# Kernel optimization log

Hardware: AMD Instinct MI355X
Metric: run time of the kernel (lower is better)

The kernel has to match this reference:

```python
import jax, jax.numpy as jnp
import numpy as np

NUM_HEADS = 16
HIDDEN = 1024
HEAD_DIM = HIDDEN // NUM_HEADS


def setup_inputs() -> dict:
    key = jax.random.key(0)
    ks = jax.random.split(key, 9)
    B, S, D = 2, 2048, HIDDEN
    s = 1.0 / np.sqrt(D)
    return {
        "x": jax.random.normal(ks[0], (B, S, D), dtype=jnp.float32),
        "Wq": jax.random.normal(ks[1], (D, D), dtype=jnp.float32) * s,
        "bq": jnp.zeros((D,), dtype=jnp.float32),
        "Wk": jax.random.normal(ks[2], (D, D), dtype=jnp.float32) * s,
        "bk": jnp.zeros((D,), dtype=jnp.float32),
        "Wv": jax.random.normal(ks[3], (D, D), dtype=jnp.float32) * s,
        "bv": jnp.zeros((D,), dtype=jnp.float32),
        "Wo": jax.random.normal(ks[4], (D, D), dtype=jnp.float32) * s,
        "bo": jnp.zeros((D,), dtype=jnp.float32),
    }


def reference(x, Wq, bq, Wk, bk, Wv, bv, Wo, bo):
    B, S, D = x.shape
    H, Hd = NUM_HEADS, HEAD_DIM
    # projections -> [B, H, S, Hd]
    def proj(W, b):
        return (x @ W + b).reshape(B, S, H, Hd).transpose(0, 2, 1, 3)
    q = proj(Wq, bq)
    k = proj(Wk, bk)
    v = proj(Wv, bv)
    scores = jnp.einsum('bhqd,bhkd->bhqk', q, k) / jnp.sqrt(jnp.float32(Hd))
    p_attn = jax.nn.softmax(scores, axis=-1)  # dropout = identity (eval)
    ctx = jnp.einsum('bhqk,bhkd->bhqd', p_attn, v)
    attn_mean = jnp.mean(p_attn, axis=1)  # [B, S, S]
    out = ctx.transpose(0, 2, 1, 3).reshape(B, S, D) @ Wo + bo
    return out, attn_mean
```

## Files before the change

kernel.cpp:

```cpp
#include <hip/hip_runtime.h>
#include <math.h>

#define NUM_HEADS 16
#define HEAD_DIM  64
#define HIDDEN    1024
#define BATCH     2
#define SEQ       2048

#define QSCALE 0.1803368801111204f

typedef short bf16x8 __attribute__((ext_vector_type(8)));
typedef short short4v __attribute__((ext_vector_type(4)));
typedef float f32x4 __attribute__((ext_vector_type(4)));

#if __has_builtin(__builtin_amdgcn_exp2f)
#define EXP2F __builtin_amdgcn_exp2f
#else
#define EXP2F exp2f
#endif

#define ACQB(N) do { asm volatile("s_waitcnt vmcnt(" #N ")" ::: "memory"); \
                     __builtin_amdgcn_s_barrier(); } while (0)
#define RELB()  do { asm volatile("s_waitcnt lgkmcnt(0)" ::: "memory");   \
                     __builtin_amdgcn_sched_barrier(0);                    \
                     __builtin_amdgcn_s_barrier(); } while (0)

__device__ __forceinline__ short f2bf(float f) {
    union { float f; unsigned int u; } x; x.f = f;
    unsigned int r = x.u + 0x7fffu + ((x.u >> 16) & 1u);
    return (short)(r >> 16);
}

__device__ __forceinline__ unsigned int pack_bf16_trunc(float lo, float hi) {
    return __builtin_amdgcn_perm(__float_as_uint(hi), __float_as_uint(lo), 0x07060302u);
}

__device__ __forceinline__ void async16(const void* g, void* l) {
    __builtin_amdgcn_global_load_lds(
        (const __attribute__((address_space(1))) void*)g,
        (__attribute__((address_space(3))) void*)l, 16, 0, 0);
}

__global__ __launch_bounds__(256)
void prep_kernel(const float* __restrict__ x,
                 const float* __restrict__ Wq, const float* __restrict__ Wk,
                 const float* __restrict__ Wv, const float* __restrict__ Wo,
                 short* __restrict__ xb, short* __restrict__ Wt4)
{
    __shared__ float t[64][65];
    const int tid = threadIdx.x;
    const int bid = blockIdx.x;
    if (bid < 4096) {
        size_t i = ((size_t)bid * 256 + tid) * 4;
        float4 v = *(const float4*)&x[i];
        short4v o;
        o.x = f2bf(v.x); o.y = f2bf(v.y); o.z = f2bf(v.z); o.w = f2bf(v.w);
        *(short4v*)&xb[i] = o;
        return;
    }
    const int tb = bid - 4096;
    const int z  = tb >> 8;
    const int cx = tb & 15, cy = (tb >> 4) & 15;
    const float* W = (z == 0) ? Wq : (z == 1) ? Wk : (z == 2) ? Wv : Wo;
    short* dst = Wt4 + (size_t)z * HIDDEN * HIDDEN;
    const int c0 = cx * 64;
    const int r0 = cy * 64;
    const int cl = tid & 63, rw = tid >> 6;
    #pragma unroll
    for (int p = 0; p < 16; ++p) {
        int row = p * 4 + rw;
        t[row][cl] = W[(size_t)(r0 + row) * HIDDEN + c0 + cl];
    }
    __syncthreads();
    #pragma unroll
    for (int p = 0; p < 16; ++p) {
        int orow = p * 4 + rw;
        dst[(size_t)(c0 + orow) * HIDDEN + r0 + cl] = f2bf(t[cl][orow]);
    }
}

__global__ __launch_bounds__(256)
void qkv_proj_kernel(const short* __restrict__ xb, const short* __restrict__ Wt4,
                     const float* __restrict__ bq, const float* __restrict__ bk,
                     const float* __restrict__ bv,
                     short* __restrict__ Qb, short* __restrict__ Kb,
                     short* __restrict__ Vt)
{
    __shared__ short ldsA[2][128 * 32];
    __shared__ short ldsB[2][128 * 32];
    const int tid = threadIdx.x;
    const int lane = tid & 63, w = tid >> 6;
    const int l = lane & 15, q = lane >> 4;
    const int n0 = blockIdx.x * 128;
    const int m0 = blockIdx.y * 128;
    const int z  = blockIdx.z;
    const short* Wt = Wt4 + (size_t)z * HIDDEN * HIDDEN;
    const int wm = (w >> 1) * 64, wn = (w & 1) * 64;
    const int kc = q ^ ((l >> 1) & 3);

    f32x4 acc[4][4];
    #pragma unroll
    for (int i = 0; i < 4; ++i)
        #pragma unroll
        for (int j = 0; j < 4; ++j)
            acc[i][j] = (f32x4){0.f, 0.f, 0.f, 0.f};

    auto STG = [&](int buf, int t) {
        #pragma unroll
        for (int half = 0; half < 2; ++half) {
            int c = half * 256 + tid;
            int row = c >> 2;
            int kcg = (c & 3) ^ ((row >> 1) & 3);
            async16(xb + (size_t)(m0 + row) * HIDDEN + t * 32 + kcg * 8, &ldsA[buf][c * 8]);
            async16(Wt + (size_t)(n0 + row) * HIDDEN + t * 32 + kcg * 8, &ldsB[buf][c * 8]);
        }
    };
    auto CMP = [&](int buf) {
        bf16x8 af[4], bfr[4];
        #pragma unroll
        for (int i = 0; i < 4; ++i)
            af[i] = *(const bf16x8*)&ldsA[buf][((wm + 16 * i + l) * 4 + kc) * 8];
        #pragma unroll
        for (int j = 0; j < 4; ++j)
            bfr[j] = *(const bf16x8*)&ldsB[buf][((wn + 16 * j + l) * 4 + kc) * 8];
        #pragma unroll
        for (int i = 0; i < 4; ++i)
            #pragma unroll
            for (int j = 0; j < 4; ++j)
                acc[i][j] = __builtin_amdgcn_mfma_f32_16x16x32_bf16(
                    af[i], bfr[j], acc[i][j], 0, 0, 0);
    };

    STG(0, 0); STG(1, 1);
    ACQB(4);
    for (int tp = 0; tp < 15; ++tp) {
        CMP(0); RELB(); STG(0, 2 * tp + 2); ACQB(4);
        CMP(1); RELB(); STG(1, 2 * tp + 3); ACQB(4);
    }
    CMP(0); RELB(); ACQB(0);
    CMP(1);

    const float* bias = (z == 0) ? bq : (z == 1) ? bk : bv;
    const float sc = (z == 0) ? QSCALE : 1.0f;
    if (z < 2) {
        short* Ob = (z == 0) ? Qb : Kb;
        #pragma unroll
        for (int j = 0; j < 4; ++j) {
            int n = n0 + wn + 16 * j + l;
            float bval = bias[n];
            int h = n >> 6, hd = n & 63;
            #pragma unroll
            for (int i = 0; i < 4; ++i) {
                #pragma unroll
                for (int reg = 0; reg < 4; ++reg) {
                    int m = m0 + wm + 16 * i + 4 * q + reg;
                    int b_ = m >> 11, s = m & 2047;
                    Ob[(((size_t)(b_ * NUM_HEADS + h) * SEQ) + s) * HEAD_DIM + hd] =
                        f2bf((acc[i][j][reg] + bval) * sc);
                }
            }
        }
    } else {
        #pragma unroll
        for (int j = 0; j < 4; ++j) {
            int n = n0 + wn + 16 * j + l;
            float bval = bias[n];
            int h = n >> 6, hd = n & 63;
            #pragma unroll
            for (int i = 0; i < 4; ++i) {
                int mb = m0 + wm + 16 * i + 4 * q;
                int b_ = mb >> 11, s = mb & 2047;
                short4v pk;
                #pragma unroll
                for (int reg = 0; reg < 4; ++reg)
                    pk[reg] = f2bf(acc[i][j][reg] + bval);
                *(short4v*)&Vt[(((size_t)(b_ * NUM_HEADS + h) * HEAD_DIM) + hd) * SEQ + s] = pk;
            }
        }
    }
}

__global__ __launch_bounds__(256)
void out_proj_kernel(const short* __restrict__ Cb, const short* __restrict__ Wot,
                     const float* __restrict__ bo, float* __restrict__ out)
{
    __shared__ short ldsA[2][64 * 32];
    __shared__ short ldsB[2][128 * 32];
    const int tid = threadIdx.x;
    const int lane = tid & 63, w = tid >> 6;
    const int l = lane & 15, q = lane >> 4;
    const int n0 = blockIdx.x * 128;
    const int m0 = blockIdx.y * 64;
    const int kc = q ^ ((l >> 1) & 3);

    f32x4 acc[4][2];
    #pragma unroll
    for (int i = 0; i < 4; ++i)
        #pragma unroll
        for (int j = 0; j < 2; ++j)
            acc[i][j] = (f32x4){0.f, 0.f, 0.f, 0.f};

    auto STG = [&](int buf, int t) {
        {
            int c = tid;
            int row = c >> 2;
            int kcg = (c & 3) ^ ((row >> 1) & 3);
            int m = m0 + row;
            int b_ = m >> 11, s = m & 2047;
            int h = t >> 1, hdb = (t & 1) << 5;
            async16(Cb + (((size_t)(b_ * NUM_HEADS + h) * SEQ) + s) * HEAD_DIM + hdb + kcg * 8,
                    &ldsA[buf][c * 8]);
        }
        #pragma unroll
        for (int half = 0; half < 2; ++half) {
            int c = half * 256 + tid;
            int row = c >> 2;
            int kcg = (c & 3) ^ ((row >> 1) & 3);
            async16(Wot + (size_t)(n0 + row) * HIDDEN + t * 32 + kcg * 8, &ldsB[buf][c * 8]);
        }
    };
    auto CMP = [&](int buf) {
        bf16x8 af[4], bfr[2];
        #pragma unroll
        for (int i = 0; i < 4; ++i)
            af[i] = *(const bf16x8*)&ldsA[buf][((16 * i + l) * 4 + kc) * 8];
        #pragma unroll
        for (int j = 0; j < 2; ++j)
            bfr[j] = *(const bf16x8*)&ldsB[buf][((32 * w + 16 * j + l) * 4 + kc) * 8];
        #pragma unroll
        for (int i = 0; i < 4; ++i)
            #pragma unroll
            for (int j = 0; j < 2; ++j)
                acc[i][j] = __builtin_amdgcn_mfma_f32_16x16x32_bf16(
                    af[i], bfr[j], acc[i][j], 0, 0, 0);
    };

    STG(0, 0); STG(1, 1);
    ACQB(3);
    for (int tp = 0; tp < 15; ++tp) {
        CMP(0); RELB(); STG(0, 2 * tp + 2); ACQB(3);
        CMP(1); RELB(); STG(1, 2 * tp + 3); ACQB(3);
    }
    CMP(0); RELB(); ACQB(0);
    CMP(1);

    #pragma unroll
    for (int j = 0; j < 2; ++j) {
        int n = n0 + 32 * w + 16 * j + l;
        float bval = bo[n];
        #pragma unroll
        for (int i = 0; i < 4; ++i)
            #pragma unroll
            for (int reg = 0; reg < 4; ++reg) {
                int m = m0 + 16 * i + 4 * q + reg;
                out[(size_t)m * HIDDEN + n] = acc[i][j][reg] + bval;
            }
    }
}

__global__ __launch_bounds__(512, 4)
void flash_kernel(const short* __restrict__ Qb, const short* __restrict__ Kb,
                  const short* __restrict__ Vt, short* __restrict__ Cb,
                  float* __restrict__ Lb)
{
    __shared__ short Ks[2][64 * 64];
    __shared__ short Vs[2][64 * 64];
    __shared__ float Xch[4][64][35];

    const int tid = threadIdx.x, lane = tid & 63, w = tid >> 6;
    const int l = lane & 15, q = lane >> 4;
    const int qg = w & 3;
    const int kh = w >> 2;
    const int q0 = blockIdx.x * 128;
    const int Q0 = q0 + qg * 32;
    const int h = blockIdx.y, b = blockIdx.z;
    const size_t base  = (size_t)(b * NUM_HEADS + h) * SEQ * HEAD_DIM;
    const size_t vbase = (size_t)(b * NUM_HEADS + h) * HEAD_DIM * SEQ;

    bf16x8 bq[2][2];
    #pragma unroll
    for (int u = 0; u < 2; ++u)
        #pragma unroll
        for (int ks = 0; ks < 2; ++ks)
            bq[u][ks] = *(const bf16x8*)(Qb + base +
                (size_t)(Q0 + 16 * u + l) * HEAD_DIM + 32 * ks + 8 * q);

    const int c = tid;
    const int row = c >> 3;
    const int g = ((c & 7) ^ (row & 7)) * 8;
    const short* kp = Kb + base + (size_t)row * HEAD_DIM + g;
    const short* vp = Vt + vbase + (size_t)row * SEQ + g;

    const int sw = l & 7;
    int kaddr[2];
    #pragma unroll
    for (int ks = 0; ks < 2; ++ks)
        kaddr[ks] = (32 * kh + l) * 64 + ((4 * ks + q) ^ sw) * 8;
    const int vc0 = 4 * kh + (q >> 1);
    const int vaddr0 = l * 64 + ((vc0      ^ sw) * 8) + 4 * (q & 1);
    const int vaddr1 = l * 64 + (((vc0 + 2) ^ sw) * 8) + 4 * (q & 1);

    f32x4 ctx[2][4];
    #pragma unroll
    for (int u = 0; u < 2; ++u)
        #pragma unroll
        for (int m = 0; m < 4; ++m) ctx[u][m] = (f32x4){0.f, 0.f, 0.f, 0.f};
    float l_part[2] = {0.f, 0.f};

    auto STG = [&](int buf) {
        async16(kp, &Ks[buf][c * 8]);
        async16(vp, &Vs[buf][c * 8]);
        kp += 64 * HEAD_DIM;
        vp += 64;
    };
    auto CMP = [&](int buf) {
        f32x4 st[2][2];
        #pragma unroll
        for (int u = 0; u < 2; ++u)
            #pragma unroll
            for (int t = 0; t < 2; ++t) st[u][t] = (f32x4){0.f, 0.f, 0.f, 0.f};
        #pragma unroll
        for (int ks = 0; ks < 2; ++ks) {
            #pragma unroll
            for (int t = 0; t < 2; ++t) {
                bf16x8 ak = *(const bf16x8*)&Ks[buf][kaddr[ks] + t * 1024];
                st[0][t] = __builtin_amdgcn_mfma_f32_16x16x32_bf16(ak, bq[0][ks], st[0][t], 0, 0, 0);
                st[1][t] = __builtin_amdgcn_mfma_f32_16x16x32_bf16(ak, bq[1][ks], st[1][t], 0, 0, 0);
            }
        }
        union { unsigned int u32[4]; bf16x8 v; } bp[2];
        #pragma unroll
        for (int u = 0; u < 2; ++u) {
            #pragma unroll
            for (int t = 0; t < 2; ++t) {
                float p0 = EXP2F(st[u][t][0]);
                float p1 = EXP2F(st[u][t][1]);
                float p2 = EXP2F(st[u][t][2]);
                float p3 = EXP2F(st[u][t][3]);
                l_part[u] += (p0 + p1) + (p2 + p3);
                bp[u].u32[2 * t]     = pack_bf16_trunc(p0, p1);
                bp[u].u32[2 * t + 1] = pack_bf16_trunc(p2, p3);
            }
        }
        #pragma unroll
        for (int m = 0; m < 4; ++m) {
            short4v g0 = *(const short4v*)&Vs[buf][vaddr0 + m * 1024];
            short4v g1 = *(const short4v*)&Vs[buf][vaddr1 + m * 1024];
            bf16x8 av = __builtin_shufflevector(g0, g1, 0, 1, 2, 3, 4, 5, 6, 7);
            ctx[0][m] = __builtin_amdgcn_mfma_f32_16x16x32_bf16(av, bp[0].v, ctx[0][m], 0, 0, 0);
            ctx[1][m] = __builtin_amdgcn_mfma_f32_16x16x32_bf16(av, bp[1].v, ctx[1][m], 0, 0, 0);
        }
    };

    STG(0); STG(1);
    ACQB(2);
    for (int tp = 0; tp < 15; ++tp) {
        CMP(0); RELB(); STG(0); ACQB(2);
        CMP(1); RELB(); STG(1); ACQB(2);
    }
    CMP(0); RELB(); ACQB(0);
    CMP(1);

    if (kh == 1) {
        float* dst = &Xch[qg][lane][0];
        #pragma unroll
        for (int u = 0; u < 2; ++u)
            #pragma unroll
            for (int m = 0; m < 4; ++m)
                #pragma unroll
                for (int r = 0; r < 4; ++r)
                    dst[u * 16 + m * 4 + r] = ctx[u][m][r];
        dst[32] = l_part[0];
        dst[33] = l_part[1];
    }
    __syncthreads();
    if (kh == 0) {
        const float* src = &Xch[qg][lane][0];
        #pragma unroll
        for (int u = 0; u < 2; ++u)
            #pragma unroll
            for (int m = 0; m < 4; ++m)
                #pragma unroll
                for (int r = 0; r < 4; ++r)
                    ctx[u][m][r] += src[u * 16 + m * 4 + r];

        #pragma unroll
        for (int u = 0; u < 2; ++u) {
            float rs = l_part[u] + src[32 + u];
            rs += __shfl_xor(rs, 16);
            rs += __shfl_xor(rs, 32);
            float inv_l = 1.0f / rs;
            int s = Q0 + 16 * u + l;
            #pragma unroll
            for (int t = 0; t < 4; ++t) {
                short4v pk;
                #pragma unroll
                for (int reg = 0; reg < 4; ++reg)
                    pk[reg] = f2bf(ctx[u][t][reg] * inv_l);
                *(short4v*)&Cb[(((size_t)(b * NUM_HEADS + h) * SEQ) + s) * HEAD_DIM + 16 * t + 4 * q] = pk;
            }
            if (q == 0)
                Lb[(size_t)(b * NUM_HEADS + h) * SEQ + s] = inv_l;
        }
    }
}

__global__ __launch_bounds__(256)
void attn_mean_kernel(const short* __restrict__ Qb, const short* __restrict__ Kb,
                      const float* __restrict__ Lb, float* __restrict__ amean)
{
    __shared__ short Qs[2][64 * 64];
    __shared__ short Ks[2][128 * 64];
    const int tid = threadIdx.x, lane = tid & 63, w = tid >> 6;
    const int l = lane & 15, q = lane >> 4;
    const int k0 = blockIdx.x * 128;
    const int q0 = blockIdx.y * 64;
    const int b  = blockIdx.z;
    const size_t HSTRIDE = (size_t)SEQ * HEAD_DIM;

    const short* qp[2];
    const short* kp[4];
    {
        const size_t base0 = (size_t)(b * NUM_HEADS) * HSTRIDE;
        #pragma unroll
        for (int i = 0; i < 2; ++i) {
            int cc = 256 * i + tid;
            int row = cc >> 3;
            int gg = ((cc & 7) ^ (row & 7)) * 8;
            qp[i] = Qb + base0 + (size_t)(q0 + row) * HEAD_DIM + gg;
        }
        #pragma unroll
        for (int i = 0; i < 4; ++i) {
            int cc = 256 * i + tid;
            int row = cc >> 3;
            int gg = ((cc & 7) ^ (row & 7)) * 8;
            kp[i] = Kb + base0 + (size_t)(k0 + row) * HEAD_DIM + gg;
        }
    }

    f32x4 macc[2][4];
    #pragma unroll
    for (int tk = 0; tk < 2; ++tk)
        #pragma unroll
        for (int tq = 0; tq < 4; ++tq)
            macc[tk][tq] = (f32x4){0.f, 0.f, 0.f, 0.f};

    auto STG = [&](int buf) {
        #pragma unroll
        for (int i = 0; i < 2; ++i) { async16(qp[i], &Qs[buf][(256 * i + tid) * 8]); qp[i] += HSTRIDE; }
        #pragma unroll
        for (int i = 0; i < 4; ++i) { async16(kp[i], &Ks[buf][(256 * i + tid) * 8]); kp[i] += HSTRIDE; }
    };
    int hc = 0;
    auto CMP = [&](int buf) {
        int h = hc++;
        float linv[4];
        #pragma unroll
        for (int tq = 0; tq < 4; ++tq)
            linv[tq] = Lb[(size_t)(b * NUM_HEADS + h) * SEQ + q0 + 16 * tq + l];

        bf16x8 bq[4][2];
        #pragma unroll
        for (int tq = 0; tq < 4; ++tq)
            #pragma unroll
            for (int ks = 0; ks < 2; ++ks) {
                int cc = (4 * ks + q) ^ (l & 7);
                bq[tq][ks] = *(const bf16x8*)&Qs[buf][((16 * tq + l) * 8 + cc) * 8];
            }
        #pragma unroll
        for (int tk = 0; tk < 2; ++tk) {
            bf16x8 ak[2];
            #pragma unroll
            for (int ks = 0; ks < 2; ++ks) {
                int cc = (4 * ks + q) ^ (l & 7);
                ak[ks] = *(const bf16x8*)&Ks[buf][((32 * w + 16 * tk + l) * 8 + cc) * 8];
            }
            #pragma unroll
            for (int tq = 0; tq < 4; ++tq) {
                f32x4 st = (f32x4){0.f, 0.f, 0.f, 0.f};
                st = __builtin_amdgcn_mfma_f32_16x16x32_bf16(ak[0], bq[tq][0], st, 0, 0, 0);
                st = __builtin_amdgcn_mfma_f32_16x16x32_bf16(ak[1], bq[tq][1], st, 0, 0, 0);
                float li = linv[tq];
                #pragma unroll
                for (int reg = 0; reg < 4; ++reg)
                    macc[tk][tq][reg] += EXP2F(st[reg]) * li;
            }
        }
    };

    STG(0); STG(1);
    ACQB(6);
    for (int tp = 0; tp < 7; ++tp) {
        CMP(0); RELB(); STG(0); ACQB(6);
        CMP(1); RELB(); STG(1); ACQB(6);
    }
    CMP(0); RELB(); ACQB(0);
    CMP(1);

    const float inv_h = 1.0f / (float)NUM_HEADS;
    #pragma unroll
    for (int tq = 0; tq < 4; ++tq) {
        int row_q = q0 + 16 * tq + l;
        #pragma unroll
        for (int tk = 0; tk < 2; ++tk) {
            int col_k = k0 + 32 * w + 16 * tk + 4 * q;
            f32x4 o;
            #pragma unroll
            for (int reg = 0; reg < 4; ++reg) o[reg] = macc[tk][tq][reg] * inv_h;
            *(f32x4*)&amean[((size_t)b * SEQ + row_q) * SEQ + col_k] = o;
        }
    }
}

extern "C" void kernel_launch(void* const* d_in, const int* in_sizes, int n_in,
                              void* d_out, int out_size, void* d_ws, size_t ws_size,
                              hipStream_t stream)
{
    const float* x  = (const float*)d_in[0];
    const float* Wq = (const float*)d_in[1];
    const float* bq = (const float*)d_in[2];
    const float* Wk = (const float*)d_in[3];
    const float* bk = (const float*)d_in[4];
    const float* Wv = (const float*)d_in[5];
    const float* bv = (const float*)d_in[6];
    const float* Wo = (const float*)d_in[7];
    const float* bo = (const float*)d_in[8];

    float* out   = (float*)d_out;
    float* amean = out + (size_t)BATCH * SEQ * HIDDEN;

    const size_t NELEM = (size_t)BATCH * NUM_HEADS * SEQ * HEAD_DIM;
    short* ws  = (short*)d_ws;
    short* xb  = ws;
    short* Wt4 = xb + NELEM;
    short* Qb  = Wt4 + 4 * (size_t)HIDDEN * HIDDEN;
    short* Kb  = Qb + NELEM;
    short* Vt  = Kb + NELEM;
    short* Cb  = Vt + NELEM;
    float* Lb  = (float*)(Cb + NELEM);

    dim3 blk(256);
    prep_kernel<<<dim3(4096 + 1024), blk, 0, stream>>>(x, Wq, Wk, Wv, Wo, xb, Wt4);
    qkv_proj_kernel<<<dim3(8, 32, 3), blk, 0, stream>>>(xb, Wt4, bq, bk, bv, Qb, Kb, Vt);
    flash_kernel<<<dim3(SEQ / 128, NUM_HEADS, BATCH), dim3(512), 0, stream>>>(Qb, Kb, Vt, Cb, Lb);
    attn_mean_kernel<<<dim3(SEQ / 128, SEQ / 64, BATCH), blk, 0, stream>>>(Qb, Kb, Lb, amean);
    out_proj_kernel<<<dim3(8, 64), blk, 0, stream>>>(Cb, Wt4 + 3 * (size_t)HIDDEN * HIDDEN, bo, out);
}
```

Measured before the change: 253.9 us.

## Merge attn-mean and out-proj into one tail kernel; deepen GEMM K-tiles

The separate attn_mean and out_proj kernels are combined into a single interleaved launch. Two of every three blocks compute attention-mean tiles and one computes output-projection tiles, so the two independent workloads overlap and one launch is removed. Both GEMMs now load 64-wide K-tiles with an 8-way XOR swizzle and a single-stage prefetch loop. The QKV grid is remapped to group tiles for better L2 reuse, and s_setprio is raised around MFMA bursts, including in flash. Flash also aliases its exchange buffer onto the K/V shared memory, which needs an added barrier.

```diff
diff --git a/kernel.cpp b/kernel.cpp
--- a/kernel.cpp
+++ b/kernel.cpp
@@ -86,17 +86,30 @@
                      short* __restrict__ Qb, short* __restrict__ Kb,
                      short* __restrict__ Vt)
 {
-    __shared__ short ldsA[2][128 * 32];
-    __shared__ short ldsB[2][128 * 32];
+    __shared__ short ldsA[2][128 * 64];
+    __shared__ short ldsB[2][128 * 64];
     const int tid = threadIdx.x;
     const int lane = tid & 63, w = tid >> 6;
     const int l = lane & 15, q = lane >> 4;
-    const int n0 = blockIdx.x * 128;
-    const int m0 = blockIdx.y * 128;
+    const int lin = blockIdx.y * 8 + blockIdx.x;
+    const int cid = (lin & 7) * 32 + (lin >> 3);
+    const int n0 = (cid & 7) * 128;
+    const int m0 = (cid >> 3) * 128;
     const int z  = blockIdx.z;
     const short* Wt = Wt4 + (size_t)z * HIDDEN * HIDDEN;
     const int wm = (w >> 1) * 64, wn = (w & 1) * 64;
-    const int kc = q ^ ((l >> 1) & 3);
+    const int sw = l & 7;
+
+    const short* pa[4]; const short* pb[4]; int ldst[4];
+    #pragma unroll
+    for (int hh = 0; hh < 4; ++hh) {
+        int c = hh * 256 + tid;
+        int row = c >> 3;
+        int kcg = (c & 7) ^ (row & 7);
+        pa[hh] = xb + (size_t)(m0 + row) * HIDDEN + kcg * 8;
+        pb[hh] = Wt + (size_t)(n0 + row) * HIDDEN + kcg * 8;
+        ldst[hh] = c * 8;
+    }
 
     f32x4 acc[4][4];
     #pragma unroll
@@ -105,39 +118,44 @@
         for (int j = 0; j < 4; ++j)
             acc[i][j] = (f32x4){0.f, 0.f, 0.f, 0.f};
 
-    auto STG = [&](int buf, int t) {
-        #pragma unroll
-        for (int half = 0; half < 2; ++half) {
-            int c = half * 256 + tid;
-            int row = c >> 2;
-            int kcg = (c & 3) ^ ((row >> 1) & 3);
-            async16(xb + (size_t)(m0 + row) * HIDDEN + t * 32 + kcg * 8, &ldsA[buf][c * 8]);
-            async16(Wt + (size_t)(n0 + row) * HIDDEN + t * 32 + kcg * 8, &ldsB[buf][c * 8]);
+    auto STG = [&](int buf) {
+        #pragma unroll
+        for (int hh = 0; hh < 4; ++hh) {
+            async16(pa[hh], &ldsA[buf][ldst[hh]]);
+            async16(pb[hh], &ldsB[buf][ldst[hh]]);
+            pa[hh] += 64; pb[hh] += 64;
         }
     };
     auto CMP = [&](int buf) {
-        bf16x8 af[4], bfr[4];
-        #pragma unroll
-        for (int i = 0; i < 4; ++i)
-            af[i] = *(const bf16x8*)&ldsA[buf][((wm + 16 * i + l) * 4 + kc) * 8];
-        #pragma unroll
-        for (int j = 0; j < 4; ++j)
-            bfr[j] = *(const bf16x8*)&ldsB[buf][((wn + 16 * j + l) * 4 + kc) * 8];
-        #pragma unroll
-        for (int i = 0; i < 4; ++i)
+        #pragma unroll
+        for (int kk = 0; kk < 2; ++kk) {
+            const int cc = ((4 * kk + q) ^ sw) * 8;
+            bf16x8 af[4], bfr[4];
+            #pragma unroll
+            for (int i = 0; i < 4; ++i)
+                af[i] = *(const bf16x8*)&ldsA[buf][(wm + 16 * i + l) * 64 + cc];
             #pragma unroll
             for (int j = 0; j < 4; ++j)
-                acc[i][j] = __builtin_amdgcn_mfma_f32_16x16x32_bf16(
-                    af[i], bfr[j], acc[i][j], 0, 0, 0);
+                bfr[j] = *(const bf16x8*)&ldsB[buf][(wn + 16 * j + l) * 64 + cc];
+            __builtin_amdgcn_s_setprio(1);
+            #pragma unroll
+            for (int i = 0; i < 4; ++i)
+                #pragma unroll
+                for (int j = 0; j < 4; ++j)
+                    acc[i][j] = __builtin_amdgcn_mfma_f32_16x16x32_bf16(
+                        af[i], bfr[j], acc[i][j], 0, 0, 0);
+            __builtin_amdgcn_s_setprio(0);
+        }
     };
 
-    STG(0, 0); STG(1, 1);
-    ACQB(4);
-    for (int tp = 0; tp < 15; ++tp) {
-        CMP(0); RELB(); STG(0, 2 * tp + 2); ACQB(4);
-        CMP(1); RELB(); STG(1, 2 * tp + 3); ACQB(4);
-    }
-    CMP(0); RELB(); ACQB(0);
+    STG(0);
+    for (int t = 0; t < 15; ++t) {
+        STG((t & 1) ^ 1);
+        ACQB(8);
+        CMP(t & 1);
+        RELB();
+    }
+    ACQB(0);
     CMP(1);
 
     const float* bias = (z == 0) ? bq : (z == 1) ? bk : bv;
@@ -180,92 +198,15 @@
     }
 }
 
-__global__ __launch_bounds__(256)
-void out_proj_kernel(const short* __restrict__ Cb, const short* __restrict__ Wot,
-                     const float* __restrict__ bo, float* __restrict__ out)
-{
-    __shared__ short ldsA[2][64 * 32];
-    __shared__ short ldsB[2][128 * 32];
-    const int tid = threadIdx.x;
-    const int lane = tid & 63, w = tid >> 6;
-    const int l = lane & 15, q = lane >> 4;
-    const int n0 = blockIdx.x * 128;
-    const int m0 = blockIdx.y * 64;
-    const int kc = q ^ ((l >> 1) & 3);
-
-    f32x4 acc[4][2];
-    #pragma unroll
-    for (int i = 0; i < 4; ++i)
-        #pragma unroll
-        for (int j = 0; j < 2; ++j)
-            acc[i][j] = (f32x4){0.f, 0.f, 0.f, 0.f};
-
-    auto STG = [&](int buf, int t) {
-        {
-            int c = tid;
-            int row = c >> 2;
-            int kcg = (c & 3) ^ ((row >> 1) & 3);
-            int m = m0 + row;
-            int b_ = m >> 11, s = m & 2047;
-            int h = t >> 1, hdb = (t & 1) << 5;
-            async16(Cb + (((size_t)(b_ * NUM_HEADS + h) * SEQ) + s) * HEAD_DIM + hdb + kcg * 8,
-                    &ldsA[buf][c * 8]);
-        }
-        #pragma unroll
-        for (int half = 0; half < 2; ++half) {
-            int c = half * 256 + tid;
-            int row = c >> 2;
-            int kcg = (c & 3) ^ ((row >> 1) & 3);
-            async16(Wot + (size_t)(n0 + row) * HIDDEN + t * 32 + kcg * 8, &ldsB[buf][c * 8]);
-        }
-    };
-    auto CMP = [&](int buf) {
-        bf16x8 af[4], bfr[2];
-        #pragma unroll
-        for (int i = 0; i < 4; ++i)
-            af[i] = *(const bf16x8*)&ldsA[buf][((16 * i + l) * 4 + kc) * 8];
-        #pragma unroll
-        for (int j = 0; j < 2; ++j)
-            bfr[j] = *(const bf16x8*)&ldsB[buf][((32 * w + 16 * j + l) * 4 + kc) * 8];
-        #pragma unroll
-        for (int i = 0; i < 4; ++i)
-            #pragma unroll
-            for (int j = 0; j < 2; ++j)
-                acc[i][j] = __builtin_amdgcn_mfma_f32_16x16x32_bf16(
-                    af[i], bfr[j], acc[i][j], 0, 0, 0);
-    };
-
-    STG(0, 0); STG(1, 1);
-    ACQB(3);
-    for (int tp = 0; tp < 15; ++tp) {
-        CMP(0); RELB(); STG(0, 2 * tp + 2); ACQB(3);
-        CMP(1); RELB(); STG(1, 2 * tp + 3); ACQB(3);
-    }
-    CMP(0); RELB(); ACQB(0);
-    CMP(1);
-
-    #pragma unroll
-    for (int j = 0; j < 2; ++j) {
-        int n = n0 + 32 * w + 16 * j + l;
-        float bval = bo[n];
-        #pragma unroll
-        for (int i = 0; i < 4; ++i)
-            #pragma unroll
-            for (int reg = 0; reg < 4; ++reg) {
-                int m = m0 + 16 * i + 4 * q + reg;
-                out[(size_t)m * HIDDEN + n] = acc[i][j][reg] + bval;
-            }
-    }
-}
-
 __global__ __launch_bounds__(512, 4)
 void flash_kernel(const short* __restrict__ Qb, const short* __restrict__ Kb,
                   const short* __restrict__ Vt, short* __restrict__ Cb,
                   float* __restrict__ Lb)
 {
-    __shared__ short Ks[2][64 * 64];
-    __shared__ short Vs[2][64 * 64];
-    __shared__ float Xch[4][64][35];
+    __shared__ __align__(16) char fsm[35840];
+    short (*Ks)[64 * 64] = (short (*)[64 * 64])fsm;
+    short (*Vs)[64 * 64] = (short (*)[64 * 64])(fsm + 16384);
+    float (*Xch)[64][35] = (float (*)[64][35])fsm;
 
     const int tid = threadIdx.x, lane = tid & 63, w = tid >> 6;
     const int l = lane & 15, q = lane >> 4;
@@ -319,6 +260,7 @@
         for (int u = 0; u < 2; ++u)
             #pragma unroll
             for (int t = 0; t < 2; ++t) st[u][t] = (f32x4){0.f, 0.f, 0.f, 0.f};
+        __builtin_amdgcn_s_setprio(1);
         #pragma unroll
         for (int ks = 0; ks < 2; ++ks) {
             #pragma unroll
@@ -328,6 +270,7 @@
                 st[1][t] = __builtin_amdgcn_mfma_f32_16x16x32_bf16(ak, bq[1][ks], st[1][t], 0, 0, 0);
             }
         }
+        __builtin_amdgcn_s_setprio(0);
         union { unsigned int u32[4]; bf16x8 v; } bp[2];
         #pragma unroll
         for (int u = 0; u < 2; ++u) {
@@ -342,6 +285,7 @@
                 bp[u].u32[2 * t + 1] = pack_bf16_trunc(p2, p3);
             }
         }
+        __builtin_amdgcn_s_setprio(1);
         #pragma unroll
         for (int m = 0; m < 4; ++m) {
             short4v g0 = *(const short4v*)&Vs[buf][vaddr0 + m * 1024];
@@ -350,6 +294,7 @@
             ctx[0][m] = __builtin_amdgcn_mfma_f32_16x16x32_bf16(av, bp[0].v, ctx[0][m], 0, 0, 0);
             ctx[1][m] = __builtin_amdgcn_mfma_f32_16x16x32_bf16(av, bp[1].v, ctx[1][m], 0, 0, 0);
         }
+        __builtin_amdgcn_s_setprio(0);
     };
 
     STG(0); STG(1);
@@ -360,6 +305,8 @@
     }
     CMP(0); RELB(); ACQB(0);
     CMP(1);
+
+    __syncthreads();
 
     if (kh == 1) {
         float* dst = &Xch[qg][lane][0];
@@ -406,108 +353,209 @@
 }
 
 __global__ __launch_bounds__(256)
-void attn_mean_kernel(const short* __restrict__ Qb, const short* __restrict__ Kb,
-                      const float* __restrict__ Lb, float* __restrict__ amean)
+void tail_kernel(const short* __restrict__ Cb, const short* __restrict__ Wot,
+                 const float* __restrict__ bo, float* __restrict__ out,
+                 const short* __restrict__ Qb, const short* __restrict__ Kb,
+                 const float* __restrict__ Lb, float* __restrict__ amean)
 {
-    __shared__ short Qs[2][64 * 64];
-    __shared__ short Ks[2][128 * 64];
+    __shared__ short smem[24576];
     const int tid = threadIdx.x, lane = tid & 63, w = tid >> 6;
     const int l = lane & 15, q = lane >> 4;
-    const int k0 = blockIdx.x * 128;
-    const int q0 = blockIdx.y * 64;
-    const int b  = blockIdx.z;
-    const size_t HSTRIDE = (size_t)SEQ * HEAD_DIM;
-
-    const short* qp[2];
-    const short* kp[4];
-    {
-        const size_t base0 = (size_t)(b * NUM_HEADS) * HSTRIDE;
-        #pragma unroll
-        for (int i = 0; i < 2; ++i) {
-            int cc = 256 * i + tid;
-            int row = cc >> 3;
-            int gg = ((cc & 7) ^ (row & 7)) * 8;
-            qp[i] = Qb + base0 + (size_t)(q0 + row) * HEAD_DIM + gg;
-        }
-        #pragma unroll
-        for (int i = 0; i < 4; ++i) {
-            int cc = 256 * i + tid;
-            int row = cc >> 3;
-            int gg = ((cc & 7) ^ (row & 7)) * 8;
-            kp[i] = Kb + base0 + (size_t)(k0 + row) * HEAD_DIM + gg;
-        }
-    }
-
-    f32x4 macc[2][4];
-    #pragma unroll
-    for (int tk = 0; tk < 2; ++tk)
-        #pragma unroll
-        for (int tq = 0; tq < 4; ++tq)
-            macc[tk][tq] = (f32x4){0.f, 0.f, 0.f, 0.f};
-
-    auto STG = [&](int buf) {
-        #pragma unroll
-        for (int i = 0; i < 2; ++i) { async16(qp[i], &Qs[buf][(256 * i + tid) * 8]); qp[i] += HSTRIDE; }
-        #pragma unroll
-        for (int i = 0; i < 4; ++i) { async16(kp[i], &Ks[buf][(256 * i + tid) * 8]); kp[i] += HSTRIDE; }
-    };
-    int hc = 0;
-    auto CMP = [&](int buf) {
-        int h = hc++;
-        float linv[4];
-        #pragma unroll
-        for (int tq = 0; tq < 4; ++tq)
-            linv[tq] = Lb[(size_t)(b * NUM_HEADS + h) * SEQ + q0 + 16 * tq + l];
-
-        bf16x8 bq[4][2];
-        #pragma unroll
-        for (int tq = 0; tq < 4; ++tq)
-            #pragma unroll
-            for (int ks = 0; ks < 2; ++ks) {
-                int cc = (4 * ks + q) ^ (l & 7);
-                bq[tq][ks] = *(const bf16x8*)&Qs[buf][((16 * tq + l) * 8 + cc) * 8];
-            }
-        #pragma unroll
-        for (int tk = 0; tk < 2; ++tk) {
-            bf16x8 ak[2];
-            #pragma unroll
-            for (int ks = 0; ks < 2; ++ks) {
-                int cc = (4 * ks + q) ^ (l & 7);
-                ak[ks] = *(const bf16x8*)&Ks[buf][((32 * w + 16 * tk + l) * 8 + cc) * 8];
-            }
-            #pragma unroll
-            for (int tq = 0; tq < 4; ++tq) {
-                f32x4 st = (f32x4){0.f, 0.f, 0.f, 0.f};
-                st = __builtin_amdgcn_mfma_f32_16x16x32_bf16(ak[0], bq[tq][0], st, 0, 0, 0);
-                st = __builtin_amdgcn_mfma_f32_16x16x32_bf16(ak[1], bq[tq][1], st, 0, 0, 0);
-                float li = linv[tq];
-                #pragma unroll
-                for (int reg = 0; reg < 4; ++reg)
-                    macc[tk][tq][reg] += EXP2F(st[reg]) * li;
-            }
-        }
-    };
-
-    STG(0); STG(1);
-    ACQB(6);
-    for (int tp = 0; tp < 7; ++tp) {
-        CMP(0); RELB(); STG(0); ACQB(6);
-        CMP(1); RELB(); STG(1); ACQB(6);
-    }
-    CMP(0); RELB(); ACQB(0);
-    CMP(1);
-
-    const float inv_h = 1.0f / (float)NUM_HEADS;
-    #pragma unroll
-    for (int tq = 0; tq < 4; ++tq) {
-        int row_q = q0 + 16 * tq + l;
-        #pragma unroll
-        for (int tk = 0; tk < 2; ++tk) {
-            int col_k = k0 + 32 * w + 16 * tk + 4 * q;
-            f32x4 o;
-            #pragma unroll
-            for (int reg = 0; reg < 4; ++reg) o[reg] = macc[tk][tq][reg] * inv_h;
-            *(f32x4*)&amean[((size_t)b * SEQ + row_q) * SEQ + col_k] = o;
+    const int sw = l & 7;
+    const int bid = blockIdx.x;
+    const int r3 = bid % 3, g3 = bid / 3;
+
+    if (r3 == 2) {
+        short (*ldsA)[64 * 64]  = (short (*)[64 * 64])smem;
+        short (*ldsB)[128 * 64] = (short (*)[128 * 64])(smem + 8192);
+        const int cid = (g3 & 7) * 64 + (g3 >> 3);
+        const int n0 = (cid & 7) * 128;
+        const int m0 = (cid >> 3) * 64;
+
+        const short* pa[2]; const short* pb[4]; int lda[2], ldb[4];
+        #pragma unroll
+        for (int hh = 0; hh < 2; ++hh) {
+            int cc = hh * 256 + tid;
+            int rowc = cc >> 3;
+            int kcg = (cc & 7) ^ (rowc & 7);
+            int m = m0 + rowc;
+            int b_ = m >> 11, s = m & 2047;
+            pa[hh] = Cb + (((size_t)(b_ * NUM_HEADS) * SEQ) + s) * HEAD_DIM + kcg * 8;
+            lda[hh] = cc * 8;
+        }
+        #pragma unroll
+        for (int hh = 0; hh < 4; ++hh) {
+            int cc = hh * 256 + tid;
+            int rowc = cc >> 3;
+            int kcg = (cc & 7) ^ (rowc & 7);
+            pb[hh] = Wot + (size_t)(n0 + rowc) * HIDDEN + kcg * 8;
+            ldb[hh] = cc * 8;
+        }
+
+        f32x4 acc[4][2];
+        #pragma unroll
+        for (int i = 0; i < 4; ++i)
+            #pragma unroll
+            for (int j = 0; j < 2; ++j)
+                acc[i][j] = (f32x4){0.f, 0.f, 0.f, 0.f};
+
+        auto STG = [&](int buf) {
+            #pragma unroll
+            for (int hh = 0; hh < 2; ++hh) {
+                async16(pa[hh], &ldsA[buf][lda[hh]]);
+                pa[hh] += (size_t)SEQ * HEAD_DIM;
+            }
+            #pragma unroll
+            for (int hh = 0; hh < 4; ++hh) {
+                async16(pb[hh], &ldsB[buf][ldb[hh]]);
+                pb[hh] += 64;
+            }
+        };
+        auto CMP = [&](int buf) {
+            #pragma unroll
+            for (int kk = 0; kk < 2; ++kk) {
+                const int cc = ((4 * kk + q) ^ sw) * 8;
+                bf16x8 af[4], bfr[2];
+                #pragma unroll
+                for (int i = 0; i < 4; ++i)
+                    af[i] = *(const bf16x8*)&ldsA[buf][(16 * i + l) * 64 + cc];
+                #pragma unroll
+                for (int j = 0; j < 2; ++j)
+                    bfr[j] = *(const bf16x8*)&ldsB[buf][(32 * w + 16 * j + l) * 64 + cc];
+                __builtin_amdgcn_s_setprio(1);
+                #pragma unroll
+                for (int i = 0; i < 4; ++i)
+                    #pragma unroll
+                    for (int j = 0; j < 2; ++j)
+                        acc[i][j] = __builtin_amdgcn_mfma_f32_16x16x32_bf16(
+                            af[i], bfr[j], acc[i][j], 0, 0, 0);
+                __builtin_amdgcn_s_setprio(0);
+            }
+        };
+
+        STG(0);
+        for (int t = 0; t < 15; ++t) {
+            STG((t & 1) ^ 1);
+            ACQB(6);
+            CMP(t & 1);
+            RELB();
+        }
+        ACQB(0);
+        CMP(1);
+
+        #pragma unroll
+        for (int j = 0; j < 2; ++j) {
+            int n = n0 + 32 * w + 16 * j + l;
+            float bval = bo[n];
+            #pragma unroll
+            for (int i = 0; i < 4; ++i)
+                #pragma unroll
+                for (int reg = 0; reg < 4; ++reg) {
+                    int m = m0 + 16 * i + 4 * q + reg;
+                    out[(size_t)m * HIDDEN + n] = acc[i][j][reg] + bval;
+                }
+        }
+    } else {
+        short (*Qs)[64 * 64]  = (short (*)[64 * 64])smem;
+        short (*Ks)[128 * 64] = (short (*)[128 * 64])(smem + 8192);
+        const int a  = g3 * 2 + r3;
+        const int k0 = (a & 15) * 128;
+        const int qy = (a >> 4) & 31;
+        const int q0 = qy * 64;
+        const int b  = a >> 9;
+        const size_t HSTRIDE = (size_t)SEQ * HEAD_DIM;
+
+        const short* qp[2];
+        const short* kp[4];
+        {
+            const size_t base0 = (size_t)(b * NUM_HEADS) * HSTRIDE;
+            #pragma unroll
+            for (int i = 0; i < 2; ++i) {
+                int cc = 256 * i + tid;
+                int rowc = cc >> 3;
+                int gg = ((cc & 7) ^ (rowc & 7)) * 8;
+                qp[i] = Qb + base0 + (size_t)(q0 + rowc) * HEAD_DIM + gg;
+            }
+            #pragma unroll
+            for (int i = 0; i < 4; ++i) {
+                int cc = 256 * i + tid;
+                int rowc = cc >> 3;
+                int gg = ((cc & 7) ^ (rowc & 7)) * 8;
+                kp[i] = Kb + base0 + (size_t)(k0 + rowc) * HEAD_DIM + gg;
+            }
+        }
+
+        f32x4 macc[2][4];
+        #pragma unroll
+        for (int tk = 0; tk < 2; ++tk)
+            #pragma unroll
+            for (int tq = 0; tq < 4; ++tq)
+                macc[tk][tq] = (f32x4){0.f, 0.f, 0.f, 0.f};
+
+        auto STG = [&](int buf) {
+            #pragma unroll
+            for (int i = 0; i < 2; ++i) { async16(qp[i], &Qs[buf][(256 * i + tid) * 8]); qp[i] += HSTRIDE; }
+            #pragma unroll
+            for (int i = 0; i < 4; ++i) { async16(kp[i], &Ks[buf][(256 * i + tid) * 8]); kp[i] += HSTRIDE; }
+        };
+        int hc = 0;
+        auto CMP = [&](int buf) {
+            int h = hc++;
+            float linv[4];
+            #pragma unroll
+            for (int tq = 0; tq < 4; ++tq)
+                linv[tq] = Lb[(size_t)(b * NUM_HEADS + h) * SEQ + q0 + 16 * tq + l];
+
+            bf16x8 bq[4][2];
+            #pragma unroll
+            for (int tq = 0; tq < 4; ++tq)
+                #pragma unroll
+                for (int ks = 0; ks < 2; ++ks) {
+                    int cc = (4 * ks + q) ^ sw;
+                    bq[tq][ks] = *(const bf16x8*)&Qs[buf][((16 * tq + l) * 8 + cc) * 8];
+                }
+            #pragma unroll
+            for (int tk = 0; tk < 2; ++tk) {
+                bf16x8 ak[2];
+                #pragma unroll
+                for (int ks = 0; ks < 2; ++ks) {
+                    int cc = (4 * ks + q) ^ sw;
+                    ak[ks] = *(const bf16x8*)&Ks[buf][((32 * w + 16 * tk + l) * 8 + cc) * 8];
+                }
+                #pragma unroll
+                for (int tq = 0; tq < 4; ++tq) {
+                    f32x4 st = (f32x4){0.f, 0.f, 0.f, 0.f};
+                    st = __builtin_amdgcn_mfma_f32_16x16x32_bf16(ak[0], bq[tq][0], st, 0, 0, 0);
+                    st = __builtin_amdgcn_mfma_f32_16x16x32_bf16(ak[1], bq[tq][1], st, 0, 0, 0);
+                    float li = linv[tq];
+                    #pragma unroll
+                    for (int reg = 0; reg < 4; ++reg)
+                        macc[tk][tq][reg] += EXP2F(st[reg]) * li;
+                }
+            }
+        };
+
+        STG(0); STG(1);
+        ACQB(6);
+        for (int tp = 0; tp < 7; ++tp) {
+            CMP(0); RELB(); STG(0); ACQB(6);
+            CMP(1); RELB(); STG(1); ACQB(6);
+        }
+        CMP(0); RELB(); ACQB(0);
+        CMP(1);
+
+        const float inv_h = 1.0f / (float)NUM_HEADS;
+        #pragma unroll
+        for (int tq = 0; tq < 4; ++tq) {
+            int row_q = q0 + 16 * tq + l;
+            #pragma unroll
+            for (int tk = 0; tk < 2; ++tk) {
+                int col_k = k0 + 32 * w + 16 * tk + 4 * q;
+                f32x4 o;
+                #pragma unroll
+                for (int reg = 0; reg < 4; ++reg) o[reg] = macc[tk][tq][reg] * inv_h;
+                *(f32x4*)&amean[((size_t)b * SEQ + row_q) * SEQ + col_k] = o;
+            }
         }
     }
 }
@@ -543,6 +591,6 @@
     prep_kernel<<<dim3(4096 + 1024), blk, 0, stream>>>(x, Wq, Wk, Wv, Wo, xb, Wt4);
     qkv_proj_kernel<<<dim3(8, 32, 3), blk, 0, stream>>>(xb, Wt4, bq, bk, bv, Qb, Kb, Vt);
     flash_kernel<<<dim3(SEQ / 128, NUM_HEADS, BATCH), dim3(512), 0, stream>>>(Qb, Kb, Vt, Cb, Lb);
-    attn_mean_kernel<<<dim3(SEQ / 128, SEQ / 64, BATCH), blk, 0, stream>>>(Qb, Kb, Lb, amean);
-    out_proj_kernel<<<dim3(8, 64), blk, 0, stream>>>(Cb, Wt4 + 3 * (size_t)HIDDEN * HIDDEN, bo, out);
-}
+    tail_kernel<<<dim3(1536), blk, 0, stream>>>(Cb, Wt4 + 3 * (size_t)HIDDEN * HIDDEN, bo, out,
+                                                Qb, Kb, Lb, amean);
+}
```

Measured after the change: 230.8 us. 1.1x faster.
